# Performance work log

Hardware: AMD Instinct MI355X
Metric: run time of the kernel (lower is better)

Reference implementation:

```python
import jax, jax.numpy as jnp
import numpy as np

SEQ, BATCH, HIDDEN = 2048, 2, 2048
N_HEADS, HEAD_DIM = 16, 128
MASK_VALUE = -10000.0


def setup_inputs() -> dict:
    key = jax.random.key(0)
    k1, k2, k3 = jax.random.split(key, 3)
    hidden_states = jax.random.normal(k1, (SEQ, BATCH, HIDDEN), jnp.float32)
    # causal mask: True where attention is NOT allowed (upper triangle)
    attention_mask = jnp.triu(jnp.ones((SEQ, SEQ), jnp.bool_), k=1)[None, None]
    w_qkv = jax.random.normal(k2, (HIDDEN, 3 * HIDDEN), jnp.float32) * (1.0 / np.sqrt(HIDDEN))
    b_qkv = jnp.zeros((3 * HIDDEN,), jnp.float32)
    w_dense = jax.random.normal(k3, (HIDDEN, HIDDEN), jnp.float32) * (1.0 / np.sqrt(HIDDEN))
    b_dense = jnp.zeros((HIDDEN,), jnp.float32)
    return {"hidden_states": hidden_states, "attention_mask": attention_mask,
            "w_qkv": w_qkv, "b_qkv": b_qkv, "w_dense": w_dense, "b_dense": b_dense}


def reference(hidden_states, attention_mask, w_qkv, b_qkv, w_dense, b_dense):
    s, b, h = hidden_states.shape
    nh, hd = N_HEADS, HEAD_DIM
    # fused QKV projection: [s,b,3h] -> [s,b,nh,3*hd] -> split
    qkv = (hidden_states @ w_qkv + b_qkv).reshape(s, b, nh, 3 * hd)
    q, k, v = jnp.split(qkv, 3, axis=-1)          # each [s,b,nh,hd]
    norm_factor = jnp.sqrt(jnp.float32(hd))
    # attention scores [b,nh,sq,sk]
    scores = jnp.einsum('sbnd,tbnd->bnst', q, k) / norm_factor
    scores = jnp.where(attention_mask, MASK_VALUE, scores)
    probs = jax.nn.softmax(scores.astype(jnp.float32), axis=-1).astype(q.dtype)
    # context [s,b,nh,hd] -> [s,b,h]
    context = jnp.einsum('bnst,tbnd->sbnd', probs, v).reshape(s, b, h)
    # RowParallelLinear with skip_bias_add: bias returned separately
    output = context @ w_dense
    return output, b_dense
```

## Files before the change

### kernel.cpp

```cpp
#include <hip/hip_runtime.h>


typedef __attribute__((ext_vector_type(8))) short bf16x8;
typedef __attribute__((ext_vector_type(4))) float f32x4;

#define MFMA_16x16x32(a, b, c) __builtin_amdgcn_mfma_f32_16x16x32_bf16(a, b, c, 0, 0, 0)

constexpr int SEQ = 2048, BATCH = 2, HID = 2048, NH = 16, HD = 128;
constexpr int MROWS = SEQ * BATCH;
constexpr int NQKV  = 3 * HID;

__device__ inline short f2bf(float f) {
    union { float f; unsigned u; } x{f};
    unsigned r = x.u + 0x7fffu + ((x.u >> 16) & 1u);
    return (short)(r >> 16);
}
__device__ inline float bf2f(short s) {
    union { unsigned u; float f; } x;
    x.u = ((unsigned)(unsigned short)s) << 16;
    return x.f;
}

__device__ __forceinline__ void async_cp16(const void* g, void* l) {
    __builtin_amdgcn_global_load_lds(
        (const __attribute__((address_space(1))) void*)g,
        (__attribute__((address_space(3))) void*)l, 16, 0, 0);
}

__global__ __launch_bounds__(256) void cvt_bf16(const float* __restrict__ src,
                                                short* __restrict__ dst)
{
    long i = ((long)blockIdx.x * 256 + threadIdx.x) * 8;
    f32x4 a = *(const f32x4*)(src + i);
    f32x4 b = *(const f32x4*)(src + i + 4);
    bf16x8 r;
    r[0]=f2bf(a[0]); r[1]=f2bf(a[1]); r[2]=f2bf(a[2]); r[3]=f2bf(a[3]);
    r[4]=f2bf(b[0]); r[5]=f2bf(b[1]); r[6]=f2bf(b[2]); r[7]=f2bf(b[3]);
    *(bf16x8*)(dst + i) = r;
}

__global__ __launch_bounds__(256) void transpose_w(const float* __restrict__ W,
                                                   short* __restrict__ Wt,
                                                   int K, int N)
{
    __shared__ __align__(16) short lsT[64 * 72];
    const int n0 = blockIdx.x * 64, k0 = blockIdx.y * 64;
    const int t = threadIdx.x;
    const int n4 = (t & 15) * 4;
#pragma unroll
    for (int s = 0; s < 4; s++) {
        int k = (t >> 4) + s * 16;
        f32x4 w = *(const f32x4*)(W + (long)(k0 + k) * N + n0 + n4);
#pragma unroll
        for (int j = 0; j < 4; j++) {
            int e = (j + (t & 3)) & 3;
            lsT[(n4 + e) * 72 + k] = f2bf(w[e]);
        }
    }
    __syncthreads();
    const int n = t >> 2, kg = (t & 3) * 16;
    *(bf16x8*)(Wt + (long)(n0 + n) * K + k0 + kg) =
        *(const bf16x8*)(lsT + n * 72 + kg);
    *(bf16x8*)(Wt + (long)(n0 + n) * K + k0 + kg + 8) =
        *(const bf16x8*)(lsT + n * 72 + kg + 8);
}

template <int MODE>
__global__ __launch_bounds__(256) void gemm_async(
    const short* __restrict__ A, const short* __restrict__ Bt,
    const float* __restrict__ bias,
    void* __restrict__ out0, short* __restrict__ dk, short* __restrict__ dv,
    int N, int K)
{
    __shared__ __align__(16) short lsA[128 * 32];
    __shared__ __align__(16) short lsB[128 * 32];

    const int tid  = threadIdx.x;
    const int lane = tid & 63;
    const int wave = tid >> 6;
    const int low4 = lane & 15;
    const int quad = lane >> 4;
    const int m0 = blockIdx.y * 128;
    const int n0 = blockIdx.x * 128;
    const int wm = (wave >> 1) * 64, wn = (wave & 1) * 64;

    f32x4 acc[4][4];
#pragma unroll
    for (int i = 0; i < 4; i++)
#pragma unroll
        for (int j = 0; j < 4; j++) acc[i][j] = (f32x4)0.0f;

    for (int k0 = 0; k0 < K; k0 += 32) {
#pragma unroll
        for (int i = 0; i < 2; i++) {
            int c = tid + i * 256;
            int row = c >> 2, c8 = c & 3;
            async_cp16(A + (long)(m0 + row) * K + k0 + c8 * 8,
                       (char*)lsA + (size_t)c * 16);
        }
#pragma unroll
        for (int i = 0; i < 2; i++) {
            int c = tid + i * 256;
            int row = c >> 2, c8 = c & 3;
            async_cp16(Bt + (long)(n0 + row) * K + k0 + c8 * 8,
                       (char*)lsB + (size_t)c * 16);
        }
        __syncthreads();

        bf16x8 af[4], bfr[4];
#pragma unroll
        for (int i = 0; i < 4; i++)
            af[i] = *(const bf16x8*)(lsA + (wm + i * 16 + low4) * 32 + quad * 8);
#pragma unroll
        for (int j = 0; j < 4; j++)
            bfr[j] = *(const bf16x8*)(lsB + (wn + j * 16 + low4) * 32 + quad * 8);
#pragma unroll
        for (int i = 0; i < 4; i++)
#pragma unroll
            for (int j = 0; j < 4; j++)
                acc[i][j] = MFMA_16x16x32(af[i], bfr[j], acc[i][j]);
        __syncthreads();
    }

#pragma unroll
    for (int i = 0; i < 4; i++) {
        int rl = wm + i * 16 + quad * 4;
#pragma unroll
        for (int j = 0; j < 4; j++) {
            int col = n0 + wn + j * 16 + low4;
#pragma unroll
            for (int r = 0; r < 4; r++) {
                int row = m0 + rl + r;
                float val = acc[i][j][r];
                if (MODE == 0) {
                    val += bias[col];
                    int head = col / 384;
                    int rem  = col - head * 384;
                    int which = rem >> 7;
                    int d = rem & 127;
                    int b = row & 1, s = row >> 1;
                    if (which == 2) {
                        dv[(((long)(b * NH + head)) * HD + d) * SEQ + s] = f2bf(val);
                    } else {
                        short* dst = (which == 0) ? (short*)out0 : dk;
                        dst[(((long)(b * NH + head)) * SEQ + s) * HD + d] = f2bf(val);
                    }
                } else {
                    ((float*)out0)[(long)row * N + col] = val;
                }
            }
        }
    }
}

__global__ __launch_bounds__(256) void flash_attn4(
    const short* __restrict__ Q, const short* __restrict__ K,
    const short* __restrict__ Vt, short* __restrict__ ctx)
{
    __shared__ __align__(16) short lsK[2][4 * 64 * 32];
    __shared__ __align__(16) short lsV[2][2 * 128 * 32];
    __shared__ __align__(16) short lsP[4 * 16 * 72];

    const int tid  = threadIdx.x;
    const int lane = tid & 63;
    const int wave = tid >> 6;
    const int low4 = lane & 15;
    const int quad = lane >> 4;
    const int bh = blockIdx.y;
    const long base = (long)bh * SEQ * HD;
    const float scale = 0.08838834764831845f;
    const int b = bh >> 4, h = bh & 15;

#pragma unroll
    for (int t = 0; t < 2; t++) {
        const int qt = (t == 0) ? (SEQ / 64 - 1 - blockIdx.x) : blockIdx.x;
        const int q0 = qt * 64;

        bf16x8 aq[4];
        {
            const short* qp = Q + base + (long)(q0 + wave * 16 + low4) * HD + quad * 8;
#pragma unroll
            for (int ds = 0; ds < 4; ds++) aq[ds] = *(const bf16x8*)(qp + ds * 32);
        }

#pragma unroll
        for (int i = 0; i < 4; i++) {
            int c = tid + i * 256;
            int dblk = c >> 8, rem = c & 255;
            int row = rem >> 2, c8 = rem & 3;
            async_cp16(K + base + (long)row * HD + dblk * 32 + c8 * 8,
                       (char*)lsK[0] + (size_t)c * 16);
        }
#pragma unroll
        for (int i = 0; i < 4; i++) {
            int c = tid + i * 256;
            int sblk = c >> 9, rem = c & 511;
            int d = rem >> 2, c8 = rem & 3;
            async_cp16(Vt + base + (long)d * SEQ + sblk * 32 + c8 * 8,
                       (char*)lsV[0] + (size_t)c * 16);
        }

        f32x4 o[8];
#pragma unroll
        for (int i = 0; i < 8; i++) o[i] = (f32x4)0.0f;
        float lsum[4] = {0.0f, 0.0f, 0.0f, 0.0f};

        __syncthreads();

        int cur = 0;
        for (int kt = 0; kt <= qt; kt++) {
            int k0 = kt * 64;

            if (kt < qt) {
                int kn = k0 + 64;
                int nxt = cur ^ 1;
#pragma unroll
                for (int i = 0; i < 4; i++) {
                    int c = tid + i * 256;
                    int dblk = c >> 8, rem = c & 255;
                    int row = rem >> 2, c8 = rem & 3;
                    async_cp16(K + base + (long)(kn + row) * HD + dblk * 32 + c8 * 8,
                               (char*)lsK[nxt] + (size_t)c * 16);
                }
#pragma unroll
                for (int i = 0; i < 4; i++) {
                    int c = tid + i * 256;
                    int sblk = c >> 9, rem = c & 511;
                    int d = rem >> 2, c8 = rem & 3;
                    async_cp16(Vt + base + (long)d * SEQ + kn + sblk * 32 + c8 * 8,
                               (char*)lsV[nxt] + (size_t)c * 16);
                }
            }

            f32x4 s[4];
#pragma unroll
            for (int nt = 0; nt < 4; nt++) s[nt] = (f32x4)0.0f;
#pragma unroll
            for (int ds = 0; ds < 4; ds++) {
#pragma unroll
                for (int nt = 0; nt < 4; nt++) {
                    bf16x8 bk = *(const bf16x8*)(lsK[cur] + ds * 2048 +
                                                 (nt * 16 + low4) * 32 + quad * 8);
                    s[nt] = MFMA_16x16x32(aq[ds], bk, s[nt]);
                }
            }

            const bool diag = (kt == qt);
            const int qi_base = q0 + wave * 16 + quad * 4;
#pragma unroll
            for (int r = 0; r < 4; r++) {
#pragma unroll
                for (int nt = 0; nt < 4; nt++) {
                    float x = s[nt][r] * scale - 16.0f;
                    if (diag) {
                        int kj = k0 + nt * 16 + low4;
                        if (kj > qi_base + r) x = -10016.0f;
                    }
                    float p = __expf(x);
                    lsum[r] += p;
                    lsP[wave * 16 * 72 + (quad * 4 + r) * 72 + nt * 16 + low4] = f2bf(p);
                }
            }

#pragma unroll
            for (int ks = 0; ks < 2; ks++) {
                bf16x8 ap = *(const bf16x8*)(lsP + wave * 16 * 72 + low4 * 72 +
                                             ks * 32 + quad * 8);
#pragma unroll
                for (int dt = 0; dt < 8; dt++) {
                    bf16x8 bv = *(const bf16x8*)(lsV[cur] + ks * 4096 +
                                                 (dt * 16 + low4) * 32 + quad * 8);
                    o[dt] = MFMA_16x16x32(ap, bv, o[dt]);
                }
            }

            __syncthreads();
            cur ^= 1;
        }

#pragma unroll
        for (int r = 0; r < 4; r++) {
            float l = lsum[r];
            for (int off = 1; off < 16; off <<= 1)
                l += __shfl_xor(l, off, 64);
            float inv = 1.0f / l;
            int srow = q0 + wave * 16 + quad * 4 + r;
#pragma unroll
            for (int dt = 0; dt < 8; dt++) {
                int d = dt * 16 + low4;
                ctx[((long)(srow * 2 + b)) * HID + h * HD + d] = f2bf(o[dt][r] * inv);
            }
        }
    }
}

__global__ __launch_bounds__(256) void copy_bias_f(const float* __restrict__ b,
                                                   float* __restrict__ out)
{
    int i = blockIdx.x * 256 + threadIdx.x;
    if (i < HID) out[i] = b[i];
}

__global__ __launch_bounds__(256) void fill_sentinel(float* __restrict__ out, int n)
{
    int i = blockIdx.x * 256 + threadIdx.x;
    if (i < n) out[i] = 12288.0f;
}

template <int MODE, typename TA>
__global__ __launch_bounds__(256) void gemm_v1(
    const TA* __restrict__ A, const float* __restrict__ B,
    const float* __restrict__ bias,
    void* __restrict__ out0, short* __restrict__ dk, short* __restrict__ dv,
    int M, int N, int K)
{
    __shared__ short lsA[128 * 40];
    __shared__ short lsB[128 * 40];

    const int tid  = threadIdx.x;
    const int lane = tid & 63;
    const int wave = tid >> 6;
    const int low4 = lane & 15;
    const int quad = lane >> 4;
    const int m0 = blockIdx.y * 128;
    const int n0 = blockIdx.x * 128;
    const int wm = (wave >> 1) * 64, wn = (wave & 1) * 64;

    f32x4 acc[4][4];
#pragma unroll
    for (int i = 0; i < 4; i++)
#pragma unroll
        for (int j = 0; j < 4; j++) acc[i][j] = (f32x4)0.0f;

    for (int k0 = 0; k0 < K; k0 += 32) {
#pragma unroll
        for (int c = 0; c < 2; c++) {
            int u = tid + c * 256;
            int row = u >> 2;
            int col = (u & 3) << 3;
            const TA* src = A + (long)(m0 + row) * K + k0 + col;
            bf16x8 r;
            if constexpr (sizeof(TA) == 4) {
                f32x4 a = *(const f32x4*)src, b = *(const f32x4*)(src + 4);
                r[0]=f2bf(a[0]); r[1]=f2bf(a[1]); r[2]=f2bf(a[2]); r[3]=f2bf(a[3]);
                r[4]=f2bf(b[0]); r[5]=f2bf(b[1]); r[6]=f2bf(b[2]); r[7]=f2bf(b[3]);
            } else {
                r = *(const bf16x8*)src;
            }
            *(bf16x8*)(lsA + row * 40 + col) = r;
        }
#pragma unroll
        for (int c = 0; c < 2; c++) {
            int u = tid + c * 256;
            int row = u >> 4;
            int col = (u & 15) << 3;
            const float* src = B + (long)(k0 + row) * N + n0 + col;
            f32x4 a = *(const f32x4*)src, b = *(const f32x4*)(src + 4);
            float vv[8] = {a[0],a[1],a[2],a[3],b[0],b[1],b[2],b[3]};
#pragma unroll
            for (int j = 0; j < 8; j++) lsB[(col + j) * 40 + row] = f2bf(vv[j]);
        }
        __syncthreads();

        bf16x8 af[4], bfr[4];
#pragma unroll
        for (int i = 0; i < 4; i++)
            af[i] = *(const bf16x8*)(lsA + (wm + i * 16 + low4) * 40 + quad * 8);
#pragma unroll
        for (int j = 0; j < 4; j++)
            bfr[j] = *(const bf16x8*)(lsB + (wn + j * 16 + low4) * 40 + quad * 8);
#pragma unroll
        for (int i = 0; i < 4; i++)
#pragma unroll
            for (int j = 0; j < 4; j++)
                acc[i][j] = MFMA_16x16x32(af[i], bfr[j], acc[i][j]);
        __syncthreads();
    }

#pragma unroll
    for (int i = 0; i < 4; i++) {
        int rl = wm + i * 16 + quad * 4;
#pragma unroll
        for (int j = 0; j < 4; j++) {
            int col = n0 + wn + j * 16 + low4;
#pragma unroll
            for (int r = 0; r < 4; r++) {
                int row = m0 + rl + r;
                float val = acc[i][j][r];
                if (MODE == 0) {
                    val += bias[col];
                    int head = col / 384;
                    int rem  = col - head * 384;
                    int which = rem >> 7;
                    int d = rem & 127;
                    int b = row & 1, s = row >> 1;
                    short* dst = (which == 0) ? (short*)out0
                                              : ((which == 1) ? dk : dv);
                    dst[(((long)(b * NH + head)) * SEQ + s) * HD + d] = f2bf(val);
                } else {
                    ((float*)out0)[(long)row * N + col] = val;
                }
            }
        }
    }
}

__global__ __launch_bounds__(256) void flash_attn_v1(
    const short* __restrict__ Q, const short* __restrict__ K,
    const short* __restrict__ V, short* __restrict__ ctx)
{
    __shared__ short lsQ[64 * 136];
    __shared__ short lsK[64 * 136];
    __shared__ short lsVt[128 * 72];
    __shared__ short lsP[4 * 16 * 72];

    const int tid  = threadIdx.x;
    const int lane = tid & 63;
    const int wave = tid >> 6;
    const int low4 = lane & 15;
    const int quad = lane >> 4;
    const int qt = blockIdx.x;
    const int bh = blockIdx.y;
    const int q0 = qt * 64;
    const long base = (long)bh * SEQ * HD;

#pragma unroll
    for (int c = 0; c < 4; c++) {
        int u = tid + c * 256;
        int row = u >> 4;
        int col = (u & 15) << 3;
        *(bf16x8*)(lsQ + row * 136 + col) =
            *(const bf16x8*)(Q + base + (long)(q0 + row) * HD + col);
    }

    f32x4 o[8];
#pragma unroll
    for (int i = 0; i < 8; i++) o[i] = (f32x4)0.0f;
    float mrow[4], lrow[4];
#pragma unroll
    for (int r = 0; r < 4; r++) { mrow[r] = -1e30f; lrow[r] = 0.0f; }

    const float scale = 0.08838834764831845f;

    for (int kt = 0; kt <= qt; kt++) {
        int k0 = kt * 64;
#pragma unroll
        for (int c = 0; c < 4; c++) {
            int u = tid + c * 256;
            int row = u >> 4;
            int col = (u & 15) << 3;
            *(bf16x8*)(lsK + row * 136 + col) =
                *(const bf16x8*)(K + base + (long)(k0 + row) * HD + col);
            bf16x8 vv = *(const bf16x8*)(V + base + (long)(k0 + row) * HD + col);
#pragma unroll
            for (int j = 0; j < 8; j++) lsVt[(col + j) * 72 + row] = vv[j];
        }
        __syncthreads();

        f32x4 s[4];
#pragma unroll
        for (int nt = 0; nt < 4; nt++) s[nt] = (f32x4)0.0f;
#pragma unroll
        for (int ds = 0; ds < 4; ds++) {
            bf16x8 aq = *(const bf16x8*)(lsQ + (wave * 16 + low4) * 136 + ds * 32 + quad * 8);
#pragma unroll
            for (int nt = 0; nt < 4; nt++) {
                bf16x8 bk = *(const bf16x8*)(lsK + (nt * 16 + low4) * 136 + ds * 32 + quad * 8);
                s[nt] = MFMA_16x16x32(aq, bk, s[nt]);
            }
        }

        int qi_base = q0 + wave * 16 + quad * 4;
#pragma unroll
        for (int r = 0; r < 4; r++) {
            int qi = qi_base + r;
            float sv[4];
            float rmax = -1e30f;
#pragma unroll
            for (int nt = 0; nt < 4; nt++) {
                int kj = k0 + nt * 16 + low4;
                float x = s[nt][r] * scale;
                if (kj > qi) x = -10000.0f;
                sv[nt] = x;
                rmax = fmaxf(rmax, x);
            }
            for (int off = 1; off < 16; off <<= 1)
                rmax = fmaxf(rmax, __shfl_xor(rmax, off, 64));
            float mnew  = fmaxf(mrow[r], rmax);
            float alpha = __expf(mrow[r] - mnew);
            float psum  = 0.0f;
#pragma unroll
            for (int nt = 0; nt < 4; nt++) {
                float p = __expf(sv[nt] - mnew);
                psum += p;
                lsP[wave * 16 * 72 + (quad * 4 + r) * 72 + nt * 16 + low4] = f2bf(p);
            }
            for (int off = 1; off < 16; off <<= 1)
                psum += __shfl_xor(psum, off, 64);
            lrow[r] = lrow[r] * alpha + psum;
            mrow[r] = mnew;
#pragma unroll
            for (int dt = 0; dt < 8; dt++) o[dt][r] *= alpha;
        }

        __syncthreads();

#pragma unroll
        for (int ks = 0; ks < 2; ks++) {
            bf16x8 ap = *(const bf16x8*)(lsP + wave * 16 * 72 + low4 * 72 + ks * 32 + quad * 8);
#pragma unroll
            for (int dt = 0; dt < 8; dt++) {
                bf16x8 bv = *(const bf16x8*)(lsVt + (dt * 16 + low4) * 72 + ks * 32 + quad * 8);
                o[dt] = MFMA_16x16x32(ap, bv, o[dt]);
            }
        }
        __syncthreads();
    }

    int b = bh >> 4, h = bh & 15;
#pragma unroll
    for (int r = 0; r < 4; r++) {
        int srow = q0 + wave * 16 + quad * 4 + r;
        float inv = 1.0f / lrow[r];
#pragma unroll
        for (int dt = 0; dt < 8; dt++) {
            int d = dt * 16 + low4;
            ctx[((long)(srow * 2 + b)) * HID + h * HD + d] = f2bf(o[dt][r] * inv);
        }
    }
}

extern "C" void kernel_launch(void* const* d_in, const int* in_sizes, int n_in,
                              void* d_out, int out_size, void* d_ws, size_t ws_size,
                              hipStream_t stream)
{
    const float* hidden  = (const float*)d_in[0];
    const float* w_qkv   = (const float*)d_in[2];
    const float* b_qkv   = (const float*)d_in[3];
    const float* w_dense = (const float*)d_in[4];
    const float* b_dense = (const float*)d_in[5];
    float* out = (float*)d_out;

    const size_t HE  = (size_t)BATCH * NH * SEQ * HD;
    const size_t WT1 = (size_t)NQKV * HID;
    const size_t fast_need = (4 * HE + WT1) * 2;
    const size_t fb_need   = 4 * HE * 2;

    dim3 blk(256);

    if (ws_size >= fast_need) {
        short* q   = (short*)d_ws;
        short* k   = q + HE;
        short* vt  = k + HE;
        short* X   = vt + HE;
        short* Wt1 = X + HE;
        short* ctx = Wt1;
        short* Wt2 = Wt1 + HE;

        cvt_bf16<<<dim3((MROWS * HID) / 2048), blk, 0, stream>>>(hidden, X);
        transpose_w<<<dim3(NQKV / 64, HID / 64), blk, 0, stream>>>(w_qkv, Wt1, HID, NQKV);
        gemm_async<0><<<dim3(NQKV / 128, MROWS / 128), blk, 0, stream>>>(
            X, Wt1, b_qkv, q, k, vt, NQKV, HID);
        transpose_w<<<dim3(HID / 64, HID / 64), blk, 0, stream>>>(w_dense, Wt2, HID, HID);
        flash_attn4<<<dim3(SEQ / 128, BATCH * NH), blk, 0, stream>>>(q, k, vt, ctx);
        gemm_async<1><<<dim3(HID / 128, MROWS / 128), blk, 0, stream>>>(
            ctx, Wt2, nullptr, out, nullptr, nullptr, HID, HID);
        copy_bias_f<<<dim3((HID + 255) / 256), blk, 0, stream>>>(
            b_dense, out + (size_t)MROWS * HID);
    } else if (ws_size >= fb_need) {
        short* q   = (short*)d_ws;
        short* k   = q + HE;
        short* v   = k + HE;
        short* ctx = v + HE;
        gemm_v1<0, float><<<dim3(NQKV / 128, MROWS / 128), blk, 0, stream>>>(
            hidden, w_qkv, b_qkv, q, k, v, MROWS, NQKV, HID);
        flash_attn_v1<<<dim3(SEQ / 64, BATCH * NH), blk, 0, stream>>>(q, k, v, ctx);
        gemm_v1<1, short><<<dim3(HID / 128, MROWS / 128), blk, 0, stream>>>(
            ctx, w_dense, nullptr, out, nullptr, nullptr, MROWS, HID, HID);
        copy_bias_f<<<dim3((HID + 255) / 256), blk, 0, stream>>>(
            b_dense, out + (size_t)MROWS * HID);
    } else {
        fill_sentinel<<<dim3((out_size + 255) / 256), blk, 0, stream>>>(out, out_size);
    }
}
```

Before: 447.8 us.

## Double GEMM k-tile to 64 with XOR-swizzled LDS layout and hoisted epilogue math

The GEMM k-step grows from 32 to 64, halving the number of loop iterations and barrier pairs per tile. LDS rows are XOR-swizzled by 16-byte chunk to avoid bank conflicts on the wider rows. The epilogue hoists the head/which/bias computation per 16-column group instead of per element. LDS use doubles to 32KB per block, which may reduce occupancy.

```diff
diff --git a/kernel.cpp b/kernel.cpp
--- a/kernel.cpp
+++ b/kernel.cpp
@@ -72,8 +72,8 @@
     void* __restrict__ out0, short* __restrict__ dk, short* __restrict__ dv,
     int N, int K)
 {
-    __shared__ __align__(16) short lsA[128 * 32];
-    __shared__ __align__(16) short lsB[128 * 32];
+    __shared__ __align__(16) short lsA[128 * 64];
+    __shared__ __align__(16) short lsB[128 * 64];
 
     const int tid  = threadIdx.x;
     const int lane = tid & 63;
@@ -90,54 +90,71 @@
 #pragma unroll
         for (int j = 0; j < 4; j++) acc[i][j] = (f32x4)0.0f;
 
-    for (int k0 = 0; k0 < K; k0 += 32) {
-#pragma unroll
-        for (int i = 0; i < 2; i++) {
+    for (int k0 = 0; k0 < K; k0 += 64) {
+#pragma unroll
+        for (int i = 0; i < 4; i++) {
             int c = tid + i * 256;
-            int row = c >> 2, c8 = c & 3;
-            async_cp16(A + (long)(m0 + row) * K + k0 + c8 * 8,
+            int row = c >> 3, c8 = c & 7;
+            int g8 = c8 ^ (row & 7);
+            async_cp16(A + (long)(m0 + row) * K + k0 + g8 * 8,
                        (char*)lsA + (size_t)c * 16);
         }
 #pragma unroll
-        for (int i = 0; i < 2; i++) {
+        for (int i = 0; i < 4; i++) {
             int c = tid + i * 256;
-            int row = c >> 2, c8 = c & 3;
-            async_cp16(Bt + (long)(n0 + row) * K + k0 + c8 * 8,
+            int row = c >> 3, c8 = c & 7;
+            int g8 = c8 ^ (row & 7);
+            async_cp16(Bt + (long)(n0 + row) * K + k0 + g8 * 8,
                        (char*)lsB + (size_t)c * 16);
         }
         __syncthreads();
 
-        bf16x8 af[4], bfr[4];
-#pragma unroll
-        for (int i = 0; i < 4; i++)
-            af[i] = *(const bf16x8*)(lsA + (wm + i * 16 + low4) * 32 + quad * 8);
-#pragma unroll
-        for (int j = 0; j < 4; j++)
-            bfr[j] = *(const bf16x8*)(lsB + (wn + j * 16 + low4) * 32 + quad * 8);
-#pragma unroll
-        for (int i = 0; i < 4; i++)
-#pragma unroll
-            for (int j = 0; j < 4; j++)
-                acc[i][j] = MFMA_16x16x32(af[i], bfr[j], acc[i][j]);
-        __syncthreads();
-    }
-
-#pragma unroll
-    for (int i = 0; i < 4; i++) {
-        int rl = wm + i * 16 + quad * 4;
-#pragma unroll
-        for (int j = 0; j < 4; j++) {
-            int col = n0 + wn + j * 16 + low4;
+#pragma unroll
+        for (int kk = 0; kk < 2; kk++) {
+            bf16x8 af[4], bfr[4];
+#pragma unroll
+            for (int i = 0; i < 4; i++) {
+                int row = wm + i * 16 + low4;
+                int ch = (quad + 4 * kk) ^ (row & 7);
+                af[i] = *(const bf16x8*)(lsA + row * 64 + ch * 8);
+            }
+#pragma unroll
+            for (int j = 0; j < 4; j++) {
+                int row = wn + j * 16 + low4;
+                int ch = (quad + 4 * kk) ^ (row & 7);
+                bfr[j] = *(const bf16x8*)(lsB + row * 64 + ch * 8);
+            }
+#pragma unroll
+            for (int i = 0; i < 4; i++)
+#pragma unroll
+                for (int j = 0; j < 4; j++)
+                    acc[i][j] = MFMA_16x16x32(af[i], bfr[j], acc[i][j]);
+        }
+        __syncthreads();
+    }
+
+#pragma unroll
+    for (int j = 0; j < 4; j++) {
+        const int col0 = n0 + wn + j * 16;
+        int head = 0, which = 0, dbase = 0;
+        float bval = 0.0f;
+        if (MODE == 0) {
+            head  = col0 / 384;
+            int rem = col0 - head * 384;
+            which = rem >> 7;
+            dbase = rem & 127;
+            bval  = bias[col0 + low4];
+        }
+#pragma unroll
+        for (int i = 0; i < 4; i++) {
+            int rl = wm + i * 16 + quad * 4;
 #pragma unroll
             for (int r = 0; r < 4; r++) {
                 int row = m0 + rl + r;
                 float val = acc[i][j][r];
                 if (MODE == 0) {
-                    val += bias[col];
-                    int head = col / 384;
-                    int rem  = col - head * 384;
-                    int which = rem >> 7;
-                    int d = rem & 127;
+                    val += bval;
+                    int d = dbase + low4;
                     int b = row & 1, s = row >> 1;
                     if (which == 2) {
                         dv[(((long)(b * NH + head)) * HD + d) * SEQ + s] = f2bf(val);
@@ -146,7 +163,7 @@
                         dst[(((long)(b * NH + head)) * SEQ + s) * HD + d] = f2bf(val);
                     }
                 } else {
-                    ((float*)out0)[(long)row * N + col] = val;
+                    ((float*)out0)[(long)row * N + col0 + low4] = val;
                 }
             }
         }
```

After: 410.4 us. -8.4%, faster.
